# Optimization experiments

Measured on AMD Instinct MI355X. Metric: run time of the kernel, lower is better.

The kernel has to match this reference:

```python
import jax, jax.numpy as jnp
import numpy as np

D_MODEL = 1024
N_HEAD = 16
D_K = D_MODEL // N_HEAD
FFN = 4096
EPS = 1e-5


def setup_inputs() -> dict:
    key = jax.random.key(0)
    ks = jax.random.split(key, 12)
    s = 0.02
    return {
        "x": jax.random.normal(ks[0], (16, 512, D_MODEL), dtype=jnp.float32),
        "ln1_g": jnp.ones((D_MODEL,), jnp.float32),
        "ln1_b": jnp.zeros((D_MODEL,), jnp.float32),
        "w_q": jax.random.normal(ks[1], (D_MODEL, D_MODEL), jnp.float32) * s,
        "w_k": jax.random.normal(ks[2], (D_MODEL, D_MODEL), jnp.float32) * s,
        "w_v": jax.random.normal(ks[3], (D_MODEL, D_MODEL), jnp.float32) * s,
        "w_o": jax.random.normal(ks[4], (D_MODEL, D_MODEL), jnp.float32) * s,
        "b_o": jnp.zeros((D_MODEL,), jnp.float32),
        "ln2_g": jnp.ones((D_MODEL,), jnp.float32),
        "ln2_b": jnp.zeros((D_MODEL,), jnp.float32),
        "w1": jax.random.normal(ks[5], (D_MODEL, FFN), jnp.float32) * s,
        "b1": jnp.zeros((FFN,), jnp.float32),
        "w2": jax.random.normal(ks[6], (FFN, D_MODEL), jnp.float32) * s,
        "b2": jnp.zeros((D_MODEL,), jnp.float32),
    }


def layernorm(x, g, b):
    mu = jnp.mean(x, axis=-1, keepdims=True)
    var = jnp.mean((x - mu) ** 2, axis=-1, keepdims=True)
    return (x - mu) * jax.lax.rsqrt(var + EPS) * g + b


def reference(x, ln1_g, ln1_b, w_q, w_k, w_v, w_o, b_o, ln2_g, ln2_b, w1, b1, w2, b2):
    B, T, C = x.shape
    # --- attention sublayer (pre-LN) ---
    h = layernorm(x, ln1_g, ln1_b)
    # torch Linear: y = x @ W.T; here weights stored as (in, out) so y = x @ W
    q = (h @ w_q).reshape(B, T, N_HEAD, D_K).transpose(0, 2, 1, 3)  # bhtd
    k = (h @ w_k).reshape(B, T, N_HEAD, D_K).transpose(0, 2, 1, 3)
    v = (h @ w_v).reshape(B, T, N_HEAD, D_K).transpose(0, 2, 1, 3)
    scale = 1.0 / jnp.sqrt(jnp.float32(D_K))
    attn = jnp.einsum("bhqd,bhkd->bhqk", q, k) * scale  # [B,H,T,T]
    causal = jnp.tril(jnp.ones((T, T), bool))
    attn = jnp.where(causal[None, None], attn, -jnp.inf)
    attn = jax.nn.softmax(attn, axis=-1)
    out = jnp.einsum("bhqk,bhkd->bhqd", attn, v)
    out = out.transpose(0, 2, 1, 3).reshape(B, T, C)
    attn_out = out @ w_o + b_o
    x = x + attn_out
    # --- FFN sublayer (pre-LN) ---
    h = layernorm(x, ln2_g, ln2_b)
    ffn_out = jax.nn.gelu(h @ w1 + b1, approximate=False) @ w2 + b2
    return x + ffn_out
```

## Files before the change

### kernel.cpp

```cpp
#include <hip/hip_runtime.h>
#include <hip/hip_bf16.h>
#include <math.h>

#define D_MODEL 1024
#define FFN_DIM 4096
#define NHEAD 16
#define DK 64
#define BATCH 16
#define SEQ 512
#define ROWS (BATCH * SEQ)
#define QKV_N 3072

typedef short short8 __attribute__((ext_vector_type(8)));
typedef float f32x4 __attribute__((ext_vector_type(4)));

__device__ __forceinline__ float bf2f(short s) {
    return __uint_as_float(((unsigned)(unsigned short)s) << 16);
}
__device__ __forceinline__ short f2bf(float f) {
    unsigned u = __float_as_uint(f);
    u += 0x7fff + ((u >> 16) & 1);
    return (short)(u >> 16);
}

__device__ __forceinline__ int swz(int row, int col) {
    int s = (row ^ (row >> 3)) & 7;
    return row * 64 + ((((col >> 3) ^ s) << 3) | (col & 7));
}

__device__ __forceinline__ void gll16(const short* g, short* l) {
    __builtin_amdgcn_global_load_lds(
        (const __attribute__((address_space(1))) unsigned int*)g,
        (__attribute__((address_space(3))) unsigned int*)l, 16, 0, 0);
}

__global__ __launch_bounds__(256) void convT(const float* __restrict__ in,
                                             short* __restrict__ out,
                                             int K, int N) {
    __shared__ short t[64 * 64];
    const int tid = threadIdx.x;
    const int k0 = blockIdx.y * 64, n0 = blockIdx.x * 64;
    {
        const int r = tid >> 4;
        const int c4 = (tid & 15) * 4;
#pragma unroll
        for (int i = 0; i < 4; ++i) {
            const int row = i * 16 + r;
            float4 vv = *(const float4*)&in[(size_t)(k0 + row) * N + n0 + c4];
            t[swz(row, c4 + 0)] = f2bf(vv.x);
            t[swz(row, c4 + 1)] = f2bf(vv.y);
            t[swz(row, c4 + 2)] = f2bf(vv.z);
            t[swz(row, c4 + 3)] = f2bf(vv.w);
        }
    }
    __syncthreads();
    {
        const int n = tid >> 2;
        const int kc = (tid & 3) * 16;
        short tmp[16];
#pragma unroll
        for (int kk = 0; kk < 16; ++kk) tmp[kk] = t[swz(kc + kk, n)];
        short8 s0, s1;
#pragma unroll
        for (int j = 0; j < 8; ++j) { s0[j] = tmp[j]; s1[j] = tmp[8 + j]; }
        short* dst = &out[(size_t)(n0 + n) * K + k0 + kc];
        *(short8*)dst = s0;
        *(short8*)(dst + 8) = s1;
    }
}

__global__ __launch_bounds__(256) void ln_kernel(const float* __restrict__ x,
                                                 const float* __restrict__ g,
                                                 const float* __restrict__ beta,
                                                 short* __restrict__ out) {
    const int row = blockIdx.x;
    const int tid = threadIdx.x;
    const float4 xv = ((const float4*)(x + (size_t)row * D_MODEL))[tid];
    float s  = xv.x + xv.y + xv.z + xv.w;
    float s2 = xv.x * xv.x + xv.y * xv.y + xv.z * xv.z + xv.w * xv.w;
#pragma unroll
    for (int off = 32; off >= 1; off >>= 1) {
        s  += __shfl_down(s, off);
        s2 += __shfl_down(s2, off);
    }
    __shared__ float red[8];
    if ((tid & 63) == 0) { red[(tid >> 6) * 2] = s; red[(tid >> 6) * 2 + 1] = s2; }
    __syncthreads();
    s  = red[0] + red[2] + red[4] + red[6];
    s2 = red[1] + red[3] + red[5] + red[7];
    const float mu  = s * (1.0f / D_MODEL);
    const float var = s2 * (1.0f / D_MODEL) - mu * mu;
    const float r   = rsqrtf(var + 1e-5f);
    const int c = tid * 4;
    short4 ov;
    ov.x = f2bf((xv.x - mu) * r * g[c + 0] + beta[c + 0]);
    ov.y = f2bf((xv.y - mu) * r * g[c + 1] + beta[c + 1]);
    ov.z = f2bf((xv.z - mu) * r * g[c + 2] + beta[c + 2]);
    ov.w = f2bf((xv.w - mu) * r * g[c + 3] + beta[c + 3]);
    *(short4*)(out + (size_t)row * D_MODEL + c) = ov;
}

template <int MODE>
__global__ __launch_bounds__(256) void gemm128(
    const short* __restrict__ A, const short* __restrict__ Bt,
    int M, int N, int K, int ldc,
    const float* __restrict__ bias, const float* __restrict__ resid,
    float* __restrict__ outf, short* __restrict__ outb) {
    __shared__ __align__(16) short As[128 * 64];
    __shared__ __align__(16) short Bs[128 * 64];
    const int tid = threadIdx.x;
    const int w = tid >> 6, lane = tid & 63;
    const int lm = lane & 15, quad = lane >> 4;
    const int m0 = blockIdx.y * 128, n0 = blockIdx.x * 128;
    const int wm = (w & 1) * 64, wn = (w >> 1) * 64;

    const int srl = lane >> 3;
    const int gch = (lane & 7) ^ srl;
    const short* gA[4];
    const short* gB[4];
    short* lA[4];
    short* lB[4];
#pragma unroll
    for (int j = 0; j < 4; ++j) {
        const int row = j * 32 + w * 8 + srl;
        gA[j] = A  + (size_t)(m0 + row) * K + gch * 8;
        gB[j] = Bt + (size_t)(n0 + row) * K + gch * 8;
        lA[j] = &As[(j * 32 + w * 8) * 64];
        lB[j] = &Bs[(j * 32 + w * 8) * 64];
    }

    f32x4 acc[4][4];
#pragma unroll
    for (int i = 0; i < 4; ++i)
#pragma unroll
        for (int j = 0; j < 4; ++j) acc[i][j] = (f32x4){0.f, 0.f, 0.f, 0.f};

    for (int k0 = 0; k0 < K; k0 += 64) {
        __syncthreads();
#pragma unroll
        for (int j = 0; j < 4; ++j) gll16(gA[j] + k0, lA[j]);
#pragma unroll
        for (int j = 0; j < 4; ++j) gll16(gB[j] + k0, lB[j]);
        __syncthreads();
#pragma unroll
        for (int kk = 0; kk < 2; ++kk) {
            short8 af[4], bfr[4];
#pragma unroll
            for (int mm = 0; mm < 4; ++mm) {
                const int row = wm + mm * 16 + lm;
                const int ch = (kk * 4 + quad) ^ (row & 7);
                af[mm] = *(short8*)&As[row * 64 + ch * 8];
            }
#pragma unroll
            for (int nn = 0; nn < 4; ++nn) {
                const int row = wn + nn * 16 + lm;
                const int ch = (kk * 4 + quad) ^ (row & 7);
                bfr[nn] = *(short8*)&Bs[row * 64 + ch * 8];
            }
#pragma unroll
            for (int mm = 0; mm < 4; ++mm)
#pragma unroll
                for (int nn = 0; nn < 4; ++nn)
                    acc[mm][nn] = __builtin_amdgcn_mfma_f32_16x16x32_bf16(
                        af[mm], bfr[nn], acc[mm][nn], 0, 0, 0);
        }
    }

#pragma unroll
    for (int mm = 0; mm < 4; ++mm)
#pragma unroll
        for (int nn = 0; nn < 4; ++nn)
#pragma unroll
            for (int r = 0; r < 4; ++r) {
                const int row = m0 + wm + mm * 16 + quad * 4 + r;
                const int col = n0 + wn + nn * 16 + lm;
                const float vv = acc[mm][nn][r];
                if (MODE == 0) {
                    outb[(size_t)row * ldc + col] = f2bf(vv);
                } else if (MODE == 1) {
                    outf[(size_t)row * ldc + col] =
                        vv + bias[col] + resid[(size_t)row * ldc + col];
                } else {
                    const float gv = vv + bias[col];
                    const float u = 0.7978845608f * gv * (1.0f + 0.044715f * gv * gv);
                    const float ge = gv / (1.0f + __expf(-2.0f * u));
                    outb[(size_t)row * ldc + col] = f2bf(ge);
                }
            }
}

__global__ __launch_bounds__(256) void attn_mfma(const short* __restrict__ qkv,
                                                 short* __restrict__ o) {
    __shared__ __align__(16) short Ks[64 * 64];
    __shared__ __align__(16) short Vt[64 * 64];
    __shared__ __align__(16) short Ps[4 * 16 * 64];

    const int tid = threadIdx.x;
    const int qt = blockIdx.x, h = blockIdx.y, b = blockIdx.z;
    const int w = tid >> 6, lane = tid & 63;
    const int lm = lane & 15, quad = lane >> 4;

    const int sj  = tid >> 2;
    const int sd0 = (tid & 3) * 16;

    short8 aq[2];
    {
        const short* qrow =
            qkv + (size_t)(b * SEQ + qt * 64 + w * 16 + lm) * QKV_N + h * DK;
#pragma unroll
        for (int kk = 0; kk < 2; ++kk) {
            short8 raw = *(const short8*)(qrow + kk * 32 + quad * 8);
            short8 sc;
#pragma unroll
            for (int j = 0; j < 8; ++j) sc[j] = f2bf(bf2f(raw[j]) * 0.125f);
            aq[kk] = sc;
        }
    }

    f32x4 accO[4];
#pragma unroll
    for (int i = 0; i < 4; ++i) accO[i] = (f32x4){0.f, 0.f, 0.f, 0.f};
    float mrow[4] = {-1e30f, -1e30f, -1e30f, -1e30f};
    float lrow[4] = {0.f, 0.f, 0.f, 0.f};

    short* pw = &Ps[w * 1024];

    for (int kt = 0; kt <= qt; ++kt) {
        __syncthreads();
        {
            const short* ksrc =
                qkv + (size_t)(b * SEQ + kt * 64 + sj) * QKV_N + D_MODEL + h * DK + sd0;
            short8 k0v = *(const short8*)ksrc;
            short8 k1v = *(const short8*)(ksrc + 8);
            *(short8*)&Ks[swz(sj, sd0)]     = k0v;
            *(short8*)&Ks[swz(sj, sd0 + 8)] = k1v;
            const short* vsrc =
                qkv + (size_t)(b * SEQ + kt * 64 + sj) * QKV_N + 2 * D_MODEL + h * DK + sd0;
            short8 v0v = *(const short8*)vsrc;
            short8 v1v = *(const short8*)(vsrc + 8);
#pragma unroll
            for (int dd = 0; dd < 8; ++dd) Vt[swz(sd0 + dd, sj)]     = v0v[dd];
#pragma unroll
            for (int dd = 0; dd < 8; ++dd) Vt[swz(sd0 + 8 + dd, sj)] = v1v[dd];
        }
        __syncthreads();

        f32x4 sacc[4];
#pragma unroll
        for (int nn = 0; nn < 4; ++nn) sacc[nn] = (f32x4){0.f, 0.f, 0.f, 0.f};
#pragma unroll
        for (int kk = 0; kk < 2; ++kk)
#pragma unroll
            for (int nn = 0; nn < 4; ++nn) {
                short8 bfrag = *(short8*)&Ks[swz(nn * 16 + lm, kk * 32 + quad * 8)];
                sacc[nn] = __builtin_amdgcn_mfma_f32_16x16x32_bf16(
                    aq[kk], bfrag, sacc[nn], 0, 0, 0);
            }

        if (kt == qt) {
#pragma unroll
            for (int nn = 0; nn < 4; ++nn) {
                const int kg = nn * 16 + lm;
#pragma unroll
                for (int r = 0; r < 4; ++r) {
                    const int qg = w * 16 + quad * 4 + r;
                    if (kg > qg) sacc[nn][r] = -1e30f;
                }
            }
        }

        float mnew[4], alpha[4], rsum[4];
#pragma unroll
        for (int r = 0; r < 4; ++r) {
            float mx = fmaxf(fmaxf(sacc[0][r], sacc[1][r]), fmaxf(sacc[2][r], sacc[3][r]));
#pragma unroll
            for (int msk = 1; msk <= 8; msk <<= 1) mx = fmaxf(mx, __shfl_xor(mx, msk));
            mnew[r] = fmaxf(mrow[r], mx);
            alpha[r] = __expf(mrow[r] - mnew[r]);
            rsum[r] = 0.f;
        }
#pragma unroll
        for (int nn = 0; nn < 4; ++nn)
#pragma unroll
            for (int r = 0; r < 4; ++r) {
                const float p = __expf(sacc[nn][r] - mnew[r]);
                sacc[nn][r] = p;
                rsum[r] += p;
            }
#pragma unroll
        for (int r = 0; r < 4; ++r) {
#pragma unroll
            for (int msk = 1; msk <= 8; msk <<= 1) rsum[r] += __shfl_xor(rsum[r], msk);
            lrow[r] = lrow[r] * alpha[r] + rsum[r];
            mrow[r] = mnew[r];
        }
#pragma unroll
        for (int nn = 0; nn < 4; ++nn)
#pragma unroll
            for (int r = 0; r < 4; ++r) accO[nn][r] *= alpha[r];

#pragma unroll
        for (int nn = 0; nn < 4; ++nn)
#pragma unroll
            for (int r = 0; r < 4; ++r)
                pw[swz(quad * 4 + r, nn * 16 + lm)] = f2bf(sacc[nn][r]);

#pragma unroll
        for (int kk = 0; kk < 2; ++kk) {
            short8 afrag = *(short8*)&pw[swz(lm, kk * 32 + quad * 8)];
#pragma unroll
            for (int nn = 0; nn < 4; ++nn) {
                short8 bfrag = *(short8*)&Vt[swz(nn * 16 + lm, kk * 32 + quad * 8)];
                accO[nn] = __builtin_amdgcn_mfma_f32_16x16x32_bf16(
                    afrag, bfrag, accO[nn], 0, 0, 0);
            }
        }
    }

#pragma unroll
    for (int r = 0; r < 4; ++r) {
        const float invl = 1.0f / lrow[r];
        const int row = b * SEQ + qt * 64 + w * 16 + quad * 4 + r;
#pragma unroll
        for (int nn = 0; nn < 4; ++nn)
            o[(size_t)row * D_MODEL + h * DK + nn * 16 + lm] = f2bf(accO[nn][r] * invl);
    }
}

extern "C" void kernel_launch(void* const* d_in, const int* in_sizes, int n_in,
                              void* d_out, int out_size, void* d_ws, size_t ws_size,
                              hipStream_t stream) {
    const float* x     = (const float*)d_in[0];
    const float* ln1_g = (const float*)d_in[1];
    const float* ln1_b = (const float*)d_in[2];
    const float* w_q   = (const float*)d_in[3];
    const float* w_k   = (const float*)d_in[4];
    const float* w_v   = (const float*)d_in[5];
    const float* w_o   = (const float*)d_in[6];
    const float* b_o   = (const float*)d_in[7];
    const float* ln2_g = (const float*)d_in[8];
    const float* ln2_b = (const float*)d_in[9];
    const float* w1    = (const float*)d_in[10];
    const float* b1    = (const float*)d_in[11];
    const float* w2    = (const float*)d_in[12];
    const float* b2    = (const float*)d_in[13];
    float* out = (float*)d_out;

    char* ws = (char*)d_ws;
    size_t off = 0;
    auto alloc = [&](size_t bytes) {
        char* p = ws + off;
        off += (bytes + 255) & ~(size_t)255;
        return p;
    };
    short* h_bf   = (short*)alloc((size_t)ROWS * D_MODEL * 2);
    short* qkv_bf = (short*)alloc((size_t)ROWS * QKV_N * 2);
    short* a_bf   = (short*)alloc((size_t)ROWS * D_MODEL * 2);
    float* x1     = (float*)alloc((size_t)ROWS * D_MODEL * 4);
    short* wqkvT  = (short*)alloc((size_t)QKV_N * D_MODEL * 2);
    short* woT    = (short*)alloc((size_t)D_MODEL * D_MODEL * 2);
    short* w1T    = (short*)alloc((size_t)D_MODEL * FFN_DIM * 2);
    short* w2T    = (short*)alloc((size_t)FFN_DIM * D_MODEL * 2);
    short* g1_bf  = qkv_bf;

    convT<<<dim3(16, 16), 256, 0, stream>>>(w_q, wqkvT, D_MODEL, D_MODEL);
    convT<<<dim3(16, 16), 256, 0, stream>>>(w_k, wqkvT + (size_t)D_MODEL * D_MODEL,
                                            D_MODEL, D_MODEL);
    convT<<<dim3(16, 16), 256, 0, stream>>>(w_v, wqkvT + (size_t)2 * D_MODEL * D_MODEL,
                                            D_MODEL, D_MODEL);
    convT<<<dim3(16, 16), 256, 0, stream>>>(w_o, woT, D_MODEL, D_MODEL);
    convT<<<dim3(64, 16), 256, 0, stream>>>(w1, w1T, D_MODEL, FFN_DIM);
    convT<<<dim3(16, 64), 256, 0, stream>>>(w2, w2T, FFN_DIM, D_MODEL);

    ln_kernel<<<ROWS, 256, 0, stream>>>(x, ln1_g, ln1_b, h_bf);

    gemm128<0><<<dim3(QKV_N / 128, ROWS / 128), 256, 0, stream>>>(
        h_bf, wqkvT, ROWS, QKV_N, D_MODEL, QKV_N,
        nullptr, nullptr, nullptr, qkv_bf);

    attn_mfma<<<dim3(SEQ / 64, NHEAD, BATCH), 256, 0, stream>>>(qkv_bf, a_bf);

    gemm128<1><<<dim3(D_MODEL / 128, ROWS / 128), 256, 0, stream>>>(
        a_bf, woT, ROWS, D_MODEL, D_MODEL, D_MODEL, b_o, x, x1, nullptr);

    ln_kernel<<<ROWS, 256, 0, stream>>>(x1, ln2_g, ln2_b, h_bf);

    gemm128<2><<<dim3(FFN_DIM / 128, ROWS / 128), 256, 0, stream>>>(
        h_bf, w1T, ROWS, FFN_DIM, D_MODEL, FFN_DIM, b1, nullptr, nullptr, g1_bf);

    gemm128<1><<<dim3(D_MODEL / 128, ROWS / 128), 256, 0, stream>>>(
        g1_bf, w2T, ROWS, D_MODEL, FFN_DIM, D_MODEL, b2, x1, out, nullptr);
}
```

Before: 530.9 us.

## Double-buffer GEMM LDS tiles and widen attention blocks to 128 queries

The GEMM kernel now ping-pongs between two LDS buffers for the A and B tiles. It prefetches the next K-slice with direct global-to-LDS loads while running MFMAs on the current one, and drops one barrier per iteration. The attention kernel now gives each block 128 query rows, with each wave handling two 16-row groups. This reuses every staged K/V tile across twice as many queries and skips fully masked row groups. In exchange, GEMM LDS use doubles to 64 KB per block, which can lower occupancy, and attention register pressure rises while the grid halves.

```diff
diff --git a/kernel.cpp b/kernel.cpp
--- a/kernel.cpp
+++ b/kernel.cpp
@@ -106,8 +106,8 @@
     int M, int N, int K, int ldc,
     const float* __restrict__ bias, const float* __restrict__ resid,
     float* __restrict__ outf, short* __restrict__ outb) {
-    __shared__ __align__(16) short As[128 * 64];
-    __shared__ __align__(16) short Bs[128 * 64];
+    __shared__ __align__(16) short As[2][128 * 64];
+    __shared__ __align__(16) short Bs[2][128 * 64];
     const int tid = threadIdx.x;
     const int w = tid >> 6, lane = tid & 63;
     const int lm = lane & 15, quad = lane >> 4;
@@ -118,15 +118,13 @@
     const int gch = (lane & 7) ^ srl;
     const short* gA[4];
     const short* gB[4];
-    short* lA[4];
-    short* lB[4];
+    int lofs[4];
 #pragma unroll
     for (int j = 0; j < 4; ++j) {
         const int row = j * 32 + w * 8 + srl;
         gA[j] = A  + (size_t)(m0 + row) * K + gch * 8;
         gB[j] = Bt + (size_t)(n0 + row) * K + gch * 8;
-        lA[j] = &As[(j * 32 + w * 8) * 64];
-        lB[j] = &Bs[(j * 32 + w * 8) * 64];
+        lofs[j] = (j * 32 + w * 8) * 64;
     }
 
     f32x4 acc[4][4];
@@ -135,13 +133,20 @@
 #pragma unroll
         for (int j = 0; j < 4; ++j) acc[i][j] = (f32x4){0.f, 0.f, 0.f, 0.f};
 
+#pragma unroll
+    for (int j = 0; j < 4; ++j) gll16(gA[j], &As[0][lofs[j]]);
+#pragma unroll
+    for (int j = 0; j < 4; ++j) gll16(gB[j], &Bs[0][lofs[j]]);
+
+    int buf = 0;
     for (int k0 = 0; k0 < K; k0 += 64) {
         __syncthreads();
-#pragma unroll
-        for (int j = 0; j < 4; ++j) gll16(gA[j] + k0, lA[j]);
-#pragma unroll
-        for (int j = 0; j < 4; ++j) gll16(gB[j] + k0, lB[j]);
-        __syncthreads();
+        if (k0 + 64 < K) {
+#pragma unroll
+            for (int j = 0; j < 4; ++j) gll16(gA[j] + k0 + 64, &As[buf ^ 1][lofs[j]]);
+#pragma unroll
+            for (int j = 0; j < 4; ++j) gll16(gB[j] + k0 + 64, &Bs[buf ^ 1][lofs[j]]);
+        }
 #pragma unroll
         for (int kk = 0; kk < 2; ++kk) {
             short8 af[4], bfr[4];
@@ -149,13 +154,13 @@
             for (int mm = 0; mm < 4; ++mm) {
                 const int row = wm + mm * 16 + lm;
                 const int ch = (kk * 4 + quad) ^ (row & 7);
-                af[mm] = *(short8*)&As[row * 64 + ch * 8];
+                af[mm] = *(short8*)&As[buf][row * 64 + ch * 8];
             }
 #pragma unroll
             for (int nn = 0; nn < 4; ++nn) {
                 const int row = wn + nn * 16 + lm;
                 const int ch = (kk * 4 + quad) ^ (row & 7);
-                bfr[nn] = *(short8*)&Bs[row * 64 + ch * 8];
+                bfr[nn] = *(short8*)&Bs[buf][row * 64 + ch * 8];
             }
 #pragma unroll
             for (int mm = 0; mm < 4; ++mm)
@@ -164,6 +169,7 @@
                     acc[mm][nn] = __builtin_amdgcn_mfma_f32_16x16x32_bf16(
                         af[mm], bfr[nn], acc[mm][nn], 0, 0, 0);
         }
+        buf ^= 1;
     }
 
 #pragma unroll
@@ -193,7 +199,7 @@
                                                  short* __restrict__ o) {
     __shared__ __align__(16) short Ks[64 * 64];
     __shared__ __align__(16) short Vt[64 * 64];
-    __shared__ __align__(16) short Ps[4 * 16 * 64];
+    __shared__ __align__(16) short Ps[4][32 * 64];
 
     const int tid = threadIdx.x;
     const int qt = blockIdx.x, h = blockIdx.y, b = blockIdx.z;
@@ -203,29 +209,36 @@
     const int sj  = tid >> 2;
     const int sd0 = (tid & 3) * 16;
 
-    short8 aq[2];
-    {
+    short8 aq[2][2];
+#pragma unroll
+    for (int m = 0; m < 2; ++m) {
         const short* qrow =
-            qkv + (size_t)(b * SEQ + qt * 64 + w * 16 + lm) * QKV_N + h * DK;
+            qkv + (size_t)(b * SEQ + qt * 128 + w * 32 + m * 16 + lm) * QKV_N + h * DK;
 #pragma unroll
         for (int kk = 0; kk < 2; ++kk) {
             short8 raw = *(const short8*)(qrow + kk * 32 + quad * 8);
             short8 sc;
 #pragma unroll
             for (int j = 0; j < 8; ++j) sc[j] = f2bf(bf2f(raw[j]) * 0.125f);
-            aq[kk] = sc;
-        }
-    }
-
-    f32x4 accO[4];
-#pragma unroll
-    for (int i = 0; i < 4; ++i) accO[i] = (f32x4){0.f, 0.f, 0.f, 0.f};
-    float mrow[4] = {-1e30f, -1e30f, -1e30f, -1e30f};
-    float lrow[4] = {0.f, 0.f, 0.f, 0.f};
-
-    short* pw = &Ps[w * 1024];
-
-    for (int kt = 0; kt <= qt; ++kt) {
+            aq[m][kk] = sc;
+        }
+    }
+
+    f32x4 accO[2][4];
+#pragma unroll
+    for (int m = 0; m < 2; ++m)
+#pragma unroll
+        for (int i = 0; i < 4; ++i) accO[m][i] = (f32x4){0.f, 0.f, 0.f, 0.f};
+    float mrow[2][4], lrow[2][4];
+#pragma unroll
+    for (int m = 0; m < 2; ++m)
+#pragma unroll
+        for (int r = 0; r < 4; ++r) { mrow[m][r] = -1e30f; lrow[m][r] = 0.f; }
+
+    short* pw = Ps[w];
+    const int ktmax = 2 * qt + 1;
+
+    for (int kt = 0; kt <= ktmax; ++kt) {
         __syncthreads();
         {
             const short* ksrc =
@@ -245,86 +258,105 @@
         }
         __syncthreads();
 
-        f32x4 sacc[4];
-#pragma unroll
-        for (int nn = 0; nn < 4; ++nn) sacc[nn] = (f32x4){0.f, 0.f, 0.f, 0.f};
-#pragma unroll
-        for (int kk = 0; kk < 2; ++kk)
-#pragma unroll
-            for (int nn = 0; nn < 4; ++nn) {
-                short8 bfrag = *(short8*)&Ks[swz(nn * 16 + lm, kk * 32 + quad * 8)];
-                sacc[nn] = __builtin_amdgcn_mfma_f32_16x16x32_bf16(
-                    aq[kk], bfrag, sacc[nn], 0, 0, 0);
-            }
-
-        if (kt == qt) {
-#pragma unroll
-            for (int nn = 0; nn < 4; ++nn) {
-                const int kg = nn * 16 + lm;
+        bool live[2];
+#pragma unroll
+        for (int m = 0; m < 2; ++m) {
+            const int rowmin = qt * 128 + w * 32 + m * 16;
+            live[m] = (kt * 64 <= rowmin + 15);
+            if (!live[m]) continue;
+            const bool needmask = (kt * 64 + 63 > rowmin);
+
+            f32x4 sacc[4];
+#pragma unroll
+            for (int nn = 0; nn < 4; ++nn) sacc[nn] = (f32x4){0.f, 0.f, 0.f, 0.f};
+#pragma unroll
+            for (int kk = 0; kk < 2; ++kk)
+#pragma unroll
+                for (int nn = 0; nn < 4; ++nn) {
+                    short8 bfrag = *(short8*)&Ks[swz(nn * 16 + lm, kk * 32 + quad * 8)];
+                    sacc[nn] = __builtin_amdgcn_mfma_f32_16x16x32_bf16(
+                        aq[m][kk], bfrag, sacc[nn], 0, 0, 0);
+                }
+
+            if (needmask) {
+#pragma unroll
+                for (int nn = 0; nn < 4; ++nn) {
+                    const int kg = kt * 64 + nn * 16 + lm;
+#pragma unroll
+                    for (int r = 0; r < 4; ++r) {
+                        const int qg = rowmin + quad * 4 + r;
+                        if (kg > qg) sacc[nn][r] = -1e30f;
+                    }
+                }
+            }
+
+            float mnew[4], alpha[4], rsum[4];
+#pragma unroll
+            for (int r = 0; r < 4; ++r) {
+                float mx = fmaxf(fmaxf(sacc[0][r], sacc[1][r]),
+                                 fmaxf(sacc[2][r], sacc[3][r]));
+#pragma unroll
+                for (int msk = 1; msk <= 8; msk <<= 1) mx = fmaxf(mx, __shfl_xor(mx, msk));
+                mnew[r] = fmaxf(mrow[m][r], mx);
+                alpha[r] = __expf(mrow[m][r] - mnew[r]);
+                rsum[r] = 0.f;
+            }
+#pragma unroll
+            for (int nn = 0; nn < 4; ++nn)
 #pragma unroll
                 for (int r = 0; r < 4; ++r) {
-                    const int qg = w * 16 + quad * 4 + r;
-                    if (kg > qg) sacc[nn][r] = -1e30f;
+                    const float p = __expf(sacc[nn][r] - mnew[r]);
+                    sacc[nn][r] = p;
+                    rsum[r] += p;
                 }
-            }
-        }
-
-        float mnew[4], alpha[4], rsum[4];
+#pragma unroll
+            for (int r = 0; r < 4; ++r) {
+#pragma unroll
+                for (int msk = 1; msk <= 8; msk <<= 1) rsum[r] += __shfl_xor(rsum[r], msk);
+                lrow[m][r] = lrow[m][r] * alpha[r] + rsum[r];
+                mrow[m][r] = mnew[r];
+            }
+#pragma unroll
+            for (int nn = 0; nn < 4; ++nn)
+#pragma unroll
+                for (int r = 0; r < 4; ++r) accO[m][nn][r] *= alpha[r];
+
+#pragma unroll
+            for (int nn = 0; nn < 4; ++nn)
+#pragma unroll
+                for (int r = 0; r < 4; ++r)
+                    pw[swz(m * 16 + quad * 4 + r, nn * 16 + lm)] = f2bf(sacc[nn][r]);
+        }
+
+#pragma unroll
+        for (int kk = 0; kk < 2; ++kk) {
+            short8 bfr[4];
+#pragma unroll
+            for (int nn = 0; nn < 4; ++nn)
+                bfr[nn] = *(short8*)&Vt[swz(nn * 16 + lm, kk * 32 + quad * 8)];
+#pragma unroll
+            for (int m = 0; m < 2; ++m) {
+                if (!live[m]) continue;
+                short8 afrag = *(short8*)&pw[swz(m * 16 + lm, kk * 32 + quad * 8)];
+#pragma unroll
+                for (int nn = 0; nn < 4; ++nn)
+                    accO[m][nn] = __builtin_amdgcn_mfma_f32_16x16x32_bf16(
+                        afrag, bfr[nn], accO[m][nn], 0, 0, 0);
+            }
+        }
+    }
+
+#pragma unroll
+    for (int m = 0; m < 2; ++m)
 #pragma unroll
         for (int r = 0; r < 4; ++r) {
-            float mx = fmaxf(fmaxf(sacc[0][r], sacc[1][r]), fmaxf(sacc[2][r], sacc[3][r]));
-#pragma unroll
-            for (int msk = 1; msk <= 8; msk <<= 1) mx = fmaxf(mx, __shfl_xor(mx, msk));
-            mnew[r] = fmaxf(mrow[r], mx);
-            alpha[r] = __expf(mrow[r] - mnew[r]);
-            rsum[r] = 0.f;
-        }
-#pragma unroll
-        for (int nn = 0; nn < 4; ++nn)
-#pragma unroll
-            for (int r = 0; r < 4; ++r) {
-                const float p = __expf(sacc[nn][r] - mnew[r]);
-                sacc[nn][r] = p;
-                rsum[r] += p;
-            }
-#pragma unroll
-        for (int r = 0; r < 4; ++r) {
-#pragma unroll
-            for (int msk = 1; msk <= 8; msk <<= 1) rsum[r] += __shfl_xor(rsum[r], msk);
-            lrow[r] = lrow[r] * alpha[r] + rsum[r];
-            mrow[r] = mnew[r];
-        }
-#pragma unroll
-        for (int nn = 0; nn < 4; ++nn)
-#pragma unroll
-            for (int r = 0; r < 4; ++r) accO[nn][r] *= alpha[r];
-
-#pragma unroll
-        for (int nn = 0; nn < 4; ++nn)
-#pragma unroll
-            for (int r = 0; r < 4; ++r)
-                pw[swz(quad * 4 + r, nn * 16 + lm)] = f2bf(sacc[nn][r]);
-
-#pragma unroll
-        for (int kk = 0; kk < 2; ++kk) {
-            short8 afrag = *(short8*)&pw[swz(lm, kk * 32 + quad * 8)];
-#pragma unroll
-            for (int nn = 0; nn < 4; ++nn) {
-                short8 bfrag = *(short8*)&Vt[swz(nn * 16 + lm, kk * 32 + quad * 8)];
-                accO[nn] = __builtin_amdgcn_mfma_f32_16x16x32_bf16(
-                    afrag, bfrag, accO[nn], 0, 0, 0);
-            }
-        }
-    }
-
-#pragma unroll
-    for (int r = 0; r < 4; ++r) {
-        const float invl = 1.0f / lrow[r];
-        const int row = b * SEQ + qt * 64 + w * 16 + quad * 4 + r;
-#pragma unroll
-        for (int nn = 0; nn < 4; ++nn)
-            o[(size_t)row * D_MODEL + h * DK + nn * 16 + lm] = f2bf(accO[nn][r] * invl);
-    }
+            const float invl = 1.0f / lrow[m][r];
+            const int row = b * SEQ + qt * 128 + w * 32 + m * 16 + quad * 4 + r;
+#pragma unroll
+            for (int nn = 0; nn < 4; ++nn)
+                o[(size_t)row * D_MODEL + h * DK + nn * 16 + lm] =
+                    f2bf(accO[m][nn][r] * invl);
+        }
 }
 
 extern "C" void kernel_launch(void* const* d_in, const int* in_sizes, int n_in,
@@ -378,7 +410,7 @@
         h_bf, wqkvT, ROWS, QKV_N, D_MODEL, QKV_N,
         nullptr, nullptr, nullptr, qkv_bf);
 
-    attn_mfma<<<dim3(SEQ / 64, NHEAD, BATCH), 256, 0, stream>>>(qkv_bf, a_bf);
+    attn_mfma<<<dim3(SEQ / 128, NHEAD, BATCH), 256, 0, stream>>>(qkv_bf, a_bf);
 
     gemm128<1><<<dim3(D_MODEL / 128, ROWS / 128), 256, 0, stream>>>(
         a_bf, woT, ROWS, D_MODEL, D_MODEL, D_MODEL, b_o, x, x1, nullptr);
```

Measured after the change: 511.6 us. 1.04x faster.
